# Kernel tuning notes

Measured on AMD Instinct MI355X. Metric: run time of the kernel, lower is better.

## Reference

```python
import jax, jax.numpy as jnp
import numpy as np
import math

# Poincare ball, curvature c=1 (fixed, requires_grad=False in source)
C = 1.0
SQC = math.sqrt(C)
EPS = 1e-15
BALL_EPS = 1e-5  # projection margin onto the open ball


def _beta(n):
    # B(n/2, 1/2) -- beta-concatenation scale from HNN++ (Shimizu et al.)
    return math.exp(math.lgamma(n / 2.0) + math.lgamma(0.5) - math.lgamma((n + 1) / 2.0))


def _project(x, axis):
    max_norm = (1.0 - BALL_EPS) / SQC
    n = jnp.linalg.norm(x, axis=axis, keepdims=True)
    return x * jnp.minimum(1.0, max_norm / jnp.maximum(n, EPS))


def _expmap0(v, axis):
    n = jnp.maximum(jnp.linalg.norm(v, axis=axis, keepdims=True), EPS)
    return _project(jnp.tanh(SQC * n) * v / (SQC * n), axis)


def _logmap0(x, axis):
    n = jnp.maximum(jnp.linalg.norm(x, axis=axis, keepdims=True), EPS)
    sn = jnp.minimum(SQC * n, 1.0 - 1e-7)
    return jnp.arctanh(sn) * x / (SQC * n)


def _hrelu(x, axis):
    # HReLU: relu in the tangent space at the origin
    return _expmap0(jax.nn.relu(_logmap0(x, axis)), axis)


def _poincare_fc(x, z, r):
    # Poincare fully-connected layer (HNN++): x [..., d_in], z [d_in, d_out], r [d_out]
    zn = jnp.maximum(jnp.linalg.norm(z, axis=0), EPS)        # [d_out]
    zu = z / zn                                               # unit columns
    cx2 = C * jnp.sum(x * x, axis=-1, keepdims=True)          # c*||x||^2
    drcr = 2.0 * SQC * r                                      # [d_out]
    # unidirectional Poincare MLR
    v = (2.0 * zn / SQC) * jnp.arcsinh(
        (2.0 * SQC * (x @ zu) * jnp.cosh(drcr) - (1.0 + cx2) * jnp.sinh(drcr))
        / jnp.maximum(1.0 - cx2, EPS)
    )
    # map generalized coordinates back onto the ball
    y = jnp.sinh(SQC * v) / SQC
    y = y / (1.0 + jnp.sqrt(1.0 + C * jnp.sum(y * y, axis=-1, keepdims=True)))
    return _project(y, -1)


def _hconv(x, z, r, k):
    # HConvolution2d: beta-concat unfold of kxk patches (man_dim = channels), then Poincare FC
    B, Cin, H, W = x.shape
    oh, ow = H - k + 1, W - k + 1
    v = _logmap0(x, axis=1) * (_beta(Cin * k * k) / _beta(Cin))
    # torch.F.unfold ordering: feature index = c*k*k + i*k + j
    patches = jnp.stack([v[:, :, i:i + oh, j:j + ow] for i in range(k) for j in range(k)], axis=2)
    p = patches.reshape(B, Cin * k * k, oh * ow)
    xp = _expmap0(p, axis=1).transpose(0, 2, 1)   # [B, L, Cin*k*k]
    out = _poincare_fc(xp, z, r)                  # [B, L, Cout]
    return out.transpose(0, 2, 1).reshape(B, -1, oh, ow)


def _hmaxpool2(x):
    # HMaxPool2d(kernel=2, stride=2): pick the patch element with max distance to origin
    # (distance is monotonic in the norm, so argmax over channel norm suffices)
    B, Cc, H, W = x.shape
    h, w = H // 2, W // 2
    xb = x.reshape(B, Cc, h, 2, w, 2).transpose(0, 2, 4, 1, 3, 5).reshape(B, h, w, Cc, 4)
    nb = jnp.sum(xb * xb, axis=3)                 # [B, h, w, 4] squared norms
    idx = jnp.argmax(nb, axis=-1)                 # [B, h, w]
    out = jnp.take_along_axis(xb, idx[..., None, None], axis=-1)[..., 0]  # [B, h, w, Cc]
    return out.transpose(0, 3, 1, 2)


def _hflatten(x):
    # ManifoldTensor.flatten(start_dim=1): beta-concatenation flatten (man_dim 1 -> last)
    B, Cin = x.shape[0], x.shape[1]
    n = x.shape[1] * x.shape[2] * x.shape[3]
    v = _logmap0(x, axis=1) * (_beta(n) / _beta(Cin))
    return _expmap0(v.reshape(B, n), axis=-1)


def setup_inputs() -> dict:
    key = jax.random.key(0)
    ks = jax.random.split(key, 12)
    B = 1024
    s = 0.05
    x = _expmap0(0.1 * jax.random.normal(ks[0], (B, 3, 32, 32), jnp.float32), axis=1)
    return {
        "x": x,
        "z1": s * jax.random.normal(ks[1], (75, 6), jnp.float32),    # 3*5*5 -> 6
        "b1": s * jax.random.normal(ks[2], (6,), jnp.float32),
        "z2": s * jax.random.normal(ks[3], (150, 16), jnp.float32),  # 6*5*5 -> 16
        "b2": s * jax.random.normal(ks[4], (16,), jnp.float32),
        "zf1": s * jax.random.normal(ks[5], (400, 120), jnp.float32),
        "bf1": s * jax.random.normal(ks[6], (120,), jnp.float32),
        "zf2": s * jax.random.normal(ks[7], (120, 84), jnp.float32),
        "bf2": s * jax.random.normal(ks[8], (84,), jnp.float32),
        "zf3": s * jax.random.normal(ks[9], (84, 10), jnp.float32),
        "bf3": s * jax.random.normal(ks[10], (10,), jnp.float32),
    }


def reference(x, z1, b1, z2, b2, zf1, bf1, zf2, bf2, zf3, bf3):
    h = _hmaxpool2(_hrelu(_hconv(x, z1, b1, 5), axis=1))    # [B,6,14,14]
    h = _hmaxpool2(_hrelu(_hconv(h, z2, b2, 5), axis=1))    # [B,16,5,5]
    h = _hflatten(h)                                         # [B,400]
    h = _hrelu(_poincare_fc(h, zf1, bf1), axis=-1)
    h = _hrelu(_poincare_fc(h, zf2, bf2), axis=-1)
    return _poincare_fc(h, zf3, bf3)                         # [B,10]
```

## Files before the change

### kernel.cpp

```cpp
#include <hip/hip_runtime.h>
#include <cmath>

#define EPSF 1e-15f
#define MAXN 0.99999f

#define OFF_ZU1  0
#define OFF_P1   512
#define OFF_ZU2  576
#define OFF_P2   3072
#define OFF_PF1  3200
#define OFF_PF2  3584
#define OFF_PF3  3904
#define OFF_BUF1 4096
#define OFF_BUF3 (OFF_BUF1 + 1204224)

__device__ __forceinline__ float fast_tanh_pos(float x) {
    float e = __expf(-2.0f * x);
    return (1.0f - e) / (1.0f + e);
}
__device__ __forceinline__ float fast_atanh01(float x) {
    return 0.5f * __logf((1.0f + x) / (1.0f - x));
}
__device__ __forceinline__ float sinh_k_asinh(float t, float k) {
    float at = fabsf(t);
    float lq = __logf(at + sqrtf(fmaf(at, at, 1.0f)));
    float p = __expf(k * lq);
    float r = 0.5f * (p - 1.0f / p);
    return t < 0.f ? -r : r;
}

__device__ __forceinline__ float wave_reduce_sum(float s) {
#pragma unroll
    for (int d = 1; d < 64; d <<= 1) s += __shfl_xor(s, d);
    return s;
}

__global__ __launch_bounds__(64) void prep_kernel(
        const float* __restrict__ z1, const float* __restrict__ r1,
        const float* __restrict__ z2, const float* __restrict__ r2,
        const float* __restrict__ zf1, const float* __restrict__ rf1,
        const float* __restrict__ zf2, const float* __restrict__ rf2,
        const float* __restrict__ zf3, const float* __restrict__ rf3,
        float* __restrict__ ws) {
    int blk = blockIdx.x, lane = threadIdx.x;
    const float* z; const float* r; int Din, Dout, o;
    float* zu = nullptr; float* par;
    if (blk < 6)        { z = z1;  r = r1;  Din = 75;  Dout = 6;   o = blk;       zu = ws + OFF_ZU1; par = ws + OFF_P1; }
    else if (blk < 22)  { z = z2;  r = r2;  Din = 150; Dout = 16;  o = blk - 6;   zu = ws + OFF_ZU2; par = ws + OFF_P2; }
    else if (blk < 142) { z = zf1; r = rf1; Din = 400; Dout = 120; o = blk - 22;  par = ws + OFF_PF1; }
    else if (blk < 226) { z = zf2; r = rf2; Din = 120; Dout = 84;  o = blk - 142; par = ws + OFF_PF2; }
    else                { z = zf3; r = rf3; Din = 84;  Dout = 10;  o = blk - 226; par = ws + OFF_PF3; }
    float s = 0.f;
    for (int f = lane; f < Din; f += 64) { float w = z[f * Dout + o]; s += w * w; }
    s = wave_reduce_sum(s);
    float zn = fmaxf(sqrtf(s), EPSF);
    if (lane == 0) {
        par[o] = zn;
        par[Dout + o]     = coshf(2.0f * r[o]);
        par[2 * Dout + o] = sinhf(2.0f * r[o]);
    }
    if (zu)
        for (int f = lane; f < Din; f += 64) zu[f * Dout + o] = z[f * Dout + o] / zn;
}

template<int N>
__device__ __forceinline__ float chain_fast(float (&a)[N], float n2,
        const float (&zn)[N], const float (&ch)[N], const float (&sh)[N]) {
    float nn = fmaxf(sqrtf(n2), EPSF);
    float t = fast_tanh_pos(nn);
    float s = t / nn * fminf(1.0f, MAXN / fmaxf(t, EPSF));
    float cx2 = (s * s) * n2;
    float denom = fmaxf(1.0f - cx2, EPSF);
    float ys2 = 0.f;
#pragma unroll
    for (int o = 0; o < N; o++) {
        float arg = (2.0f * (s * a[o]) * ch[o] - (1.0f + cx2) * sh[o]) / denom;
        float yy = sinh_k_asinh(arg, 2.0f * zn[o]);
        a[o] = yy; ys2 += yy * yy;
    }
    float dnm = 1.0f + sqrtf(1.0f + ys2);
    float ny2 = ys2 / (dnm * dnm);
    float ny = fmaxf(sqrtf(ny2), EPSF);
    float pf = fminf(1.0f, MAXN / ny);
    float sc = pf / dnm;
    float n2b = pf * pf * ny2;
    float nb = fmaxf(sqrtf(n2b), EPSF);
    float fb = fast_atanh01(fminf(nb, 1.0f - 1e-7f)) / nb;
    float m2 = 0.f;
#pragma unroll
    for (int o = 0; o < N; o++) { float uu = fmaxf(fb * sc * a[o], 0.f); a[o] = uu; m2 += uu * uu; }
    float m = fmaxf(sqrtf(m2), EPSF);
    float tm = fast_tanh_pos(m);
    float g = tm / m * fminf(1.0f, MAXN / fmaxf(tm, EPSF));
#pragma unroll
    for (int o = 0; o < N; o++) a[o] *= g;
    return g * g * m2;
}

__global__ __launch_bounds__(256) void conv1_kernel(const float* __restrict__ x,
        const float* __restrict__ ws, float* __restrict__ out, float ratio) {
    __shared__ float xv[3168];
    int b = blockIdx.x, tid = threadIdx.x;
    const float* zug  = ws + OFF_ZU1;
    const float* parg = ws + OFF_P1;
    for (int i = tid; i < 3072; i += 256) {
        int c = i >> 10, rem = i & 1023;
        xv[c * 1056 + (rem >> 5) * 33 + (rem & 31)] = x[(size_t)b * 3072 + i];
    }
    __syncthreads();
    for (int p = tid; p < 1024; p += 256) {
        int base = (p >> 5) * 33 + (p & 31);
        float a0 = xv[base], a1 = xv[1056 + base], a2 = xv[2112 + base];
        float n2 = a0 * a0 + a1 * a1 + a2 * a2;
        float nn = fmaxf(sqrtf(n2), EPSF);
        float f = fast_atanh01(fminf(nn, 1.0f - 1e-7f)) / nn * ratio;
        xv[base] = a0 * f; xv[1056 + base] = a1 * f; xv[2112 + base] = a2 * f;
    }
    __syncthreads();
    if (tid >= 196) return;
    int ph = tid / 14, pw = tid % 14;
    int base0 = (2 * ph) * 33 + 2 * pw;
    float acc[4][6], n2w[4];
#pragma unroll
    for (int wi = 0; wi < 4; wi++) {
        n2w[wi] = 0.f;
#pragma unroll
        for (int o = 0; o < 6; o++) acc[wi][o] = 0.f;
    }
#pragma unroll 1
    for (int c = 0; c < 3; c++) {
        float px[6][6];
#pragma unroll
        for (int r = 0; r < 6; r++)
#pragma unroll
        for (int j = 0; j < 6; j++)
            px[r][j] = xv[c * 1056 + base0 + r * 33 + j];
#pragma unroll
        for (int fi = 0; fi < 5; fi++) {
            const float* zp = zug + (c * 5 + fi) * 30;
#pragma unroll
            for (int fj = 0; fj < 5; fj++) {
                float zw[6];
#pragma unroll
                for (int o = 0; o < 6; o++) zw[o] = zp[fj * 6 + o];
#pragma unroll
                for (int dy = 0; dy < 2; dy++)
#pragma unroll
                for (int dx = 0; dx < 2; dx++) {
                    float v = px[fi + dy][fj + dx];
                    int wi = dy * 2 + dx;
                    n2w[wi] = fmaf(v, v, n2w[wi]);
#pragma unroll
                    for (int o = 0; o < 6; o++) acc[wi][o] = fmaf(v, zw[o], acc[wi][o]);
                }
            }
        }
    }
    float zn[6], chv[6], shv[6];
#pragma unroll
    for (int o = 0; o < 6; o++) { zn[o] = parg[o]; chv[o] = parg[6 + o]; shv[o] = parg[12 + o]; }
    float best[6]; float bestn = -1.f;
#pragma unroll
    for (int wi = 0; wi < 4; wi++) {
        float hn2 = chain_fast<6>(acc[wi], n2w[wi], zn, chv, shv);
        if (hn2 > bestn) {
            bestn = hn2;
#pragma unroll
            for (int o = 0; o < 6; o++) best[o] = acc[wi][o];
        }
    }
    float* op = out + (size_t)b * 1176 + tid;
#pragma unroll
    for (int o = 0; o < 6; o++) op[o * 196] = best[o];
}

__global__ __launch_bounds__(128) void conv2_kernel(const float* __restrict__ in,
        const float* __restrict__ ws, float* __restrict__ out,
        float ratio2, float ratio3) {
    __shared__ float xv[2522];
    int b0 = blockIdx.x * 2, tid = threadIdx.x;
    const float* zug  = ws + OFF_ZU2;
    const float* parg = ws + OFF_P2;
    for (int i = tid; i < 2352; i += 128) {
        int img = i / 1176, rem = i % 1176;
        int c = rem / 196, pix = rem % 196;
        xv[img * 1261 + c * 210 + (pix / 14) * 15 + pix % 14] = in[(size_t)b0 * 1176 + i];
    }
    __syncthreads();
    for (int t = tid; t < 392; t += 128) {
        int img = t / 196, pix = t % 196;
        int base = img * 1261 + (pix / 14) * 15 + pix % 14;
        float a[6]; float n2 = 0.f;
#pragma unroll
        for (int c = 0; c < 6; c++) { float v = xv[base + c * 210]; a[c] = v; n2 += v * v; }
        float nn = fmaxf(sqrtf(n2), EPSF);
        float f = fast_atanh01(fminf(nn, 1.0f - 1e-7f)) / nn * ratio2;
#pragma unroll
        for (int c = 0; c < 6; c++) xv[base + c * 210] = a[c] * f;
    }
    __syncthreads();
    int img = tid >> 6, l = tid & 63;
    int cell = l >> 1, h = l & 1;
    bool act = cell < 25;
    float best[8];
    float bestn = -1.f;
    float fcell = 0.f, part = 0.f;
    if (act) {
        int base0 = img * 1261 + (2 * (cell / 5)) * 15 + 2 * (cell % 5);
        float acc[4][8], n2w[4];
#pragma unroll
        for (int wi = 0; wi < 4; wi++) {
            n2w[wi] = 0.f;
#pragma unroll
            for (int o = 0; o < 8; o++) acc[wi][o] = 0.f;
        }
#pragma unroll 1
        for (int c = 0; c < 6; c++) {
            float px[6][6];
#pragma unroll
            for (int r = 0; r < 6; r++)
#pragma unroll
            for (int j = 0; j < 6; j++)
                px[r][j] = xv[base0 + c * 210 + r * 15 + j];
#pragma unroll
            for (int fi = 0; fi < 5; fi++) {
                const float* zp = zug + (c * 5 + fi) * 80 + 8 * h;
#pragma unroll
                for (int fj = 0; fj < 5; fj++) {
                    float zw[8];
#pragma unroll
                    for (int o = 0; o < 8; o++) zw[o] = zp[fj * 16 + o];
#pragma unroll
                    for (int dy = 0; dy < 2; dy++)
#pragma unroll
                    for (int dx = 0; dx < 2; dx++) {
                        float v = px[fi + dy][fj + dx];
                        int wi = dy * 2 + dx;
                        n2w[wi] = fmaf(v, v, n2w[wi]);
#pragma unroll
                        for (int o = 0; o < 8; o++) acc[wi][o] = fmaf(v, zw[o], acc[wi][o]);
                    }
                }
            }
        }
        float zn[8], chv[8], shv[8];
#pragma unroll
        for (int o = 0; o < 8; o++) {
            zn[o]  = parg[8 * h + o];
            chv[o] = parg[16 + 8 * h + o];
            shv[o] = parg[32 + 8 * h + o];
        }
#pragma unroll
        for (int wi = 0; wi < 4; wi++) {
            float nn = fmaxf(sqrtf(n2w[wi]), EPSF);
            float t = fast_tanh_pos(nn);
            float s = t / nn * fminf(1.0f, MAXN / fmaxf(t, EPSF));
            float cx2 = (s * s) * n2w[wi];
            float denom = fmaxf(1.0f - cx2, EPSF);
            float ys2h = 0.f;
#pragma unroll
            for (int o = 0; o < 8; o++) {
                float arg = (2.0f * (s * acc[wi][o]) * chv[o] - (1.0f + cx2) * shv[o]) / denom;
                float yy = sinh_k_asinh(arg, 2.0f * zn[o]);
                acc[wi][o] = yy; ys2h += yy * yy;
            }
            float ys2 = ys2h + __shfl_xor(ys2h, 1);
            float dnm = 1.0f + sqrtf(1.0f + ys2);
            float ny2 = ys2 / (dnm * dnm);
            float ny = fmaxf(sqrtf(ny2), EPSF);
            float pf = fminf(1.0f, MAXN / ny);
            float sc = pf / dnm;
            float n2b = pf * pf * ny2;
            float nb = fmaxf(sqrtf(n2b), EPSF);
            float fb = fast_atanh01(fminf(nb, 1.0f - 1e-7f)) / nb;
            float m2h = 0.f;
#pragma unroll
            for (int o = 0; o < 8; o++) { float uu = fmaxf(fb * sc * acc[wi][o], 0.f); acc[wi][o] = uu; m2h += uu * uu; }
            float m2 = m2h + __shfl_xor(m2h, 1);
            float m = fmaxf(sqrtf(m2), EPSF);
            float tm = fast_tanh_pos(m);
            float g = tm / m * fminf(1.0f, MAXN / fmaxf(tm, EPSF));
            float hn2 = g * g * m2;
            if (hn2 > bestn) {
                bestn = hn2;
#pragma unroll
                for (int o = 0; o < 8; o++) best[o] = g * acc[wi][o];
            }
        }
        float nn = fmaxf(sqrtf(bestn), EPSF);
        fcell = fast_atanh01(fminf(nn, 1.0f - 1e-7f)) / nn * ratio3;
        if (h == 0) part = fcell * fcell * bestn;
    }
    float s = wave_reduce_sum(part);
    float nn = fmaxf(sqrtf(s), EPSF);
    float t = fast_tanh_pos(nn);
    float g = t / nn * fminf(1.0f, MAXN / fmaxf(t, EPSF));
    if (act) {
        float* op = out + (size_t)(b0 + img) * 400 + cell;
#pragma unroll
        for (int o = 0; o < 8; o++) op[(8 * h + o) * 25] = g * fcell * best[o];
    }
}

template<int DIN, int DOUT>
__device__ __forceinline__ float dot_col(const float* __restrict__ xr,
        const float* __restrict__ z, int col) {
    float a0 = 0.f, a1 = 0.f, a2 = 0.f, a3 = 0.f;
    for (int f = 0; f < DIN; f += 4) {
        a0 = fmaf(xr[f],     z[(f)     * DOUT + col], a0);
        a1 = fmaf(xr[f + 1], z[(f + 1) * DOUT + col], a1);
        a2 = fmaf(xr[f + 2], z[(f + 2) * DOUT + col], a2);
        a3 = fmaf(xr[f + 3], z[(f + 3) * DOUT + col], a3);
    }
    return (a0 + a1) + (a2 + a3);
}

template<int DIN, int DOUT, bool RELU>
__device__ __forceinline__ float fc_layer_wave(int lane, const float* __restrict__ xr,
        float cx2, const float* __restrict__ z, const float* __restrict__ par,
        float* __restrict__ dst) {
    int o0 = lane, o1 = lane + 64;
    bool v0 = o0 < DOUT, v1 = o1 < DOUT;
    int c0 = v0 ? o0 : 0, c1 = v1 ? o1 : 0;
    float d0 = dot_col<DIN, DOUT>(xr, z, c0);
    float d1 = (DOUT > 64) ? dot_col<DIN, DOUT>(xr, z, c1) : 0.f;
    float denom = fmaxf(1.0f - cx2, EPSF);
    float zn0 = par[c0], ch0 = par[DOUT + c0], sh0 = par[2 * DOUT + c0];
    float arg0 = (2.0f * (d0 / zn0) * ch0 - (1.0f + cx2) * sh0) / denom;
    float y0 = sinh_k_asinh(arg0, 2.0f * zn0);
    float y1 = 0.f;
    if (DOUT > 64) {
        float zn1 = par[c1], ch1 = par[DOUT + c1], sh1 = par[2 * DOUT + c1];
        float arg1 = (2.0f * (d1 / zn1) * ch1 - (1.0f + cx2) * sh1) / denom;
        y1 = sinh_k_asinh(arg1, 2.0f * zn1);
    }
    float ys2 = wave_reduce_sum((v0 ? y0 * y0 : 0.f) + (v1 ? y1 * y1 : 0.f));
    float dnm = 1.0f + sqrtf(1.0f + ys2);
    float ny2 = ys2 / (dnm * dnm);
    float ny = fmaxf(sqrtf(ny2), EPSF);
    float pf = fminf(1.0f, MAXN / ny);
    float sc = pf / dnm;
    if (!RELU) {
        if (v0) dst[o0] = sc * y0;
        if (DOUT > 64 && v1) dst[o1] = sc * y1;
        return pf * pf * ny2;
    }
    float n2b = pf * pf * ny2;
    float nb = fmaxf(sqrtf(n2b), EPSF);
    float fb = fast_atanh01(fminf(nb, 1.0f - 1e-7f)) / nb;
    float u0 = fmaxf(fb * sc * y0, 0.f);
    float u1 = fmaxf(fb * sc * y1, 0.f);
    float m2 = wave_reduce_sum((v0 ? u0 * u0 : 0.f) + (v1 ? u1 * u1 : 0.f));
    float m = fmaxf(sqrtf(m2), EPSF);
    float tm = fast_tanh_pos(m);
    float g = tm / m * fminf(1.0f, MAXN / fmaxf(tm, EPSF));
    if (v0) dst[o0] = g * u0;
    if (DOUT > 64 && v1) dst[o1] = g * u1;
    return g * g * m2;
}

__global__ __launch_bounds__(256) void fc_stack_kernel(const float* __restrict__ in,
        const float* __restrict__ zf1, const float* __restrict__ zf2,
        const float* __restrict__ zf3, const float* __restrict__ ws,
        float* __restrict__ out) {
    __shared__ float xs[4][400];
    __shared__ float h1[4][120];
    __shared__ float h2[4][84];
    int wid = threadIdx.x >> 6, lane = threadIdx.x & 63;
    int b = blockIdx.x * 4 + wid;
    float* xr = xs[wid];
    float p = 0.f;
    for (int j = lane; j < 400; j += 64) { float v = in[(size_t)b * 400 + j]; xr[j] = v; p += v * v; }
    float cx2 = wave_reduce_sum(p);
    __syncthreads();
    float cx2b = fc_layer_wave<400, 120, true >(lane, xr,      cx2,  zf1, ws + OFF_PF1, h1[wid]);
    __syncthreads();
    float cx2c = fc_layer_wave<120, 84,  true >(lane, h1[wid], cx2b, zf2, ws + OFF_PF2, h2[wid]);
    __syncthreads();
    fc_layer_wave<84, 10, false>(lane, h2[wid], cx2c, zf3, ws + OFF_PF3, out + (size_t)b * 10);
}

static double beta_fn(double n) {
    return exp(lgamma(n / 2.0) + lgamma(0.5) - lgamma((n + 1) / 2.0));
}

extern "C" void kernel_launch(void* const* d_in, const int* in_sizes, int n_in,
                              void* d_out, int out_size, void* d_ws, size_t ws_size,
                              hipStream_t stream) {
    (void)in_sizes; (void)n_in; (void)out_size; (void)ws_size;
    const float* x   = (const float*)d_in[0];
    const float* z1  = (const float*)d_in[1];
    const float* b1  = (const float*)d_in[2];
    const float* z2  = (const float*)d_in[3];
    const float* b2  = (const float*)d_in[4];
    const float* zf1 = (const float*)d_in[5];
    const float* bf1 = (const float*)d_in[6];
    const float* zf2 = (const float*)d_in[7];
    const float* bf2 = (const float*)d_in[8];
    const float* zf3 = (const float*)d_in[9];
    const float* bf3 = (const float*)d_in[10];
    float* out = (float*)d_out;
    float* ws  = (float*)d_ws;

    const float ratio1 = (float)(beta_fn(75.0)  / beta_fn(3.0));
    const float ratio2 = (float)(beta_fn(150.0) / beta_fn(6.0));
    const float ratio3 = (float)(beta_fn(400.0) / beta_fn(16.0));

    float* buf1 = ws + OFF_BUF1;
    float* buf3 = ws + OFF_BUF3;

    prep_kernel<<<236, 64, 0, stream>>>(z1, b1, z2, b2, zf1, bf1, zf2, bf2, zf3, bf3, ws);
    conv1_kernel<<<1024, 256, 0, stream>>>(x, ws, buf1, ratio1);
    conv2_kernel<<<512, 128, 0, stream>>>(buf1, ws, buf3, ratio2, ratio3);
    fc_stack_kernel<<<256, 256, 0, stream>>>(buf3, zf1, zf2, zf3, ws, out);
}
```

Baseline: 182.9 us.

## Fuse conv1, conv2 and FC stack into one per-image mega kernel

Replaces the three-kernel pipeline (conv1, conv2, fc_stack) with a single kernel that processes one image per 256-thread block, keeping intermediates in shared memory instead of global buffers. Conv2 is restructured so each thread computes one output channel across a row of ten positions, with patch norms computed from precomputed row sums, and z2 staged in LDS. The FC layers now use the whole block with block-level reductions instead of one wave per image. This removes global round-trips and two launches, at the cost of larger LDS usage per block, more syncthreads, and lower parallelism in the FC phase (one image per block).

Result: faster. 175.8 us (-3.9%).

```diff
diff --git a/kernel.cpp b/kernel.cpp
--- a/kernel.cpp
+++ b/kernel.cpp
@@ -11,8 +11,6 @@
 #define OFF_PF1  3200
 #define OFF_PF2  3584
 #define OFF_PF3  3904
-#define OFF_BUF1 4096
-#define OFF_BUF3 (OFF_BUF1 + 1204224)
 
 __device__ __forceinline__ float fast_tanh_pos(float x) {
     float e = __expf(-2.0f * x);
@@ -33,6 +31,14 @@
 #pragma unroll
     for (int d = 1; d < 64; d <<= 1) s += __shfl_xor(s, d);
     return s;
+}
+
+__device__ __forceinline__ float block_reduce(float v, float* rbuf, int tid) {
+    float s = wave_reduce_sum(v);
+    __syncthreads();
+    if ((tid & 63) == 0) rbuf[tid >> 6] = s;
+    __syncthreads();
+    return rbuf[0] + rbuf[1] + rbuf[2] + rbuf[3];
 }
 
 __global__ __launch_bounds__(64) void prep_kernel(
@@ -97,139 +103,119 @@
     return g * g * m2;
 }
 
-__global__ __launch_bounds__(256) void conv1_kernel(const float* __restrict__ x,
-        const float* __restrict__ ws, float* __restrict__ out, float ratio) {
+template<int DIN, int DOUT, bool RELU>
+__device__ __forceinline__ float fc_block(int tid, const float* __restrict__ xin,
+        float gin, float cx2, const float* __restrict__ zg,
+        const float* __restrict__ parw, float* __restrict__ dst,
+        float* rbuf, float& gnext) {
+    constexpr int H = DIN / 2;
+    int col = tid >> 1, half = tid & 1;
+    bool act = tid < 2 * DOUT;
+    float d = 0.f;
+    if (act) {
+        float a0 = 0.f, a1 = 0.f;
+        int f0 = half * H;
+        for (int f = f0; f < f0 + H; f += 2) {
+            a0 = fmaf(xin[f],     zg[f * DOUT + col],       a0);
+            a1 = fmaf(xin[f + 1], zg[(f + 1) * DOUT + col], a1);
+        }
+        d = a0 + a1;
+    }
+    d += __shfl_xor(d, 1);
+    d *= gin;
+    float y = 0.f;
+    float denom = fmaxf(1.0f - cx2, EPSF);
+    if (act) {
+        float zn = parw[col], chv = parw[DOUT + col], shv = parw[2 * DOUT + col];
+        float arg = (2.0f * (d / zn) * chv - (1.0f + cx2) * shv) / denom;
+        y = sinh_k_asinh(arg, 2.0f * zn);
+    }
+    float ys2 = block_reduce((act && half == 0) ? y * y : 0.f, rbuf, tid);
+    float dnm = 1.0f + sqrtf(1.0f + ys2);
+    float ny2 = ys2 / (dnm * dnm);
+    float ny = fmaxf(sqrtf(ny2), EPSF);
+    float pf = fminf(1.0f, MAXN / ny);
+    float sc = pf / dnm;
+    if (!RELU) {
+        if (act && half == 0) dst[col] = sc * y;
+        gnext = 1.f;
+        return 0.f;
+    }
+    float n2b = pf * pf * ny2;
+    float nb = fmaxf(sqrtf(n2b), EPSF);
+    float fb = fast_atanh01(fminf(nb, 1.0f - 1e-7f)) / nb;
+    float u = fmaxf(fb * sc * y, 0.f);
+    if (act && half == 0) dst[col] = u;
+    float m2 = block_reduce((act && half == 0) ? u * u : 0.f, rbuf, tid);
+    float m = fmaxf(sqrtf(m2), EPSF);
+    float tm = fast_tanh_pos(m);
+    float g = tm / m * fminf(1.0f, MAXN / fmaxf(tm, EPSF));
+    gnext = g;
+    return g * g * m2;
+}
+
+__global__ __launch_bounds__(256) void mega_kernel(const float* __restrict__ x,
+        const float* __restrict__ ws, const float* __restrict__ zf1,
+        const float* __restrict__ zf2, const float* __restrict__ zf3,
+        float* __restrict__ out, float ratio1, float ratio2, float ratio3) {
     __shared__ float xv[3168];
+    __shared__ float z2s[2400];
+    __shared__ float par2[48];
+    __shared__ float v2[1260];
+    __shared__ float rs[140];
+    __shared__ float u3[400];
+    __shared__ float h1[120];
+    __shared__ float h2[84];
+    __shared__ float spart[5];
+    __shared__ float rbuf[4];
     int b = blockIdx.x, tid = threadIdx.x;
-    const float* zug  = ws + OFF_ZU1;
-    const float* parg = ws + OFF_P1;
+
     for (int i = tid; i < 3072; i += 256) {
         int c = i >> 10, rem = i & 1023;
         xv[c * 1056 + (rem >> 5) * 33 + (rem & 31)] = x[(size_t)b * 3072 + i];
     }
-    __syncthreads();
+    for (int i = tid; i < 2400; i += 256) z2s[i] = ws[OFF_ZU2 + i];
+    if (tid < 48) par2[tid] = ws[OFF_P2 + tid];
+    __syncthreads();
+
     for (int p = tid; p < 1024; p += 256) {
         int base = (p >> 5) * 33 + (p & 31);
         float a0 = xv[base], a1 = xv[1056 + base], a2 = xv[2112 + base];
         float n2 = a0 * a0 + a1 * a1 + a2 * a2;
         float nn = fmaxf(sqrtf(n2), EPSF);
-        float f = fast_atanh01(fminf(nn, 1.0f - 1e-7f)) / nn * ratio;
+        float f = fast_atanh01(fminf(nn, 1.0f - 1e-7f)) / nn * ratio1;
         xv[base] = a0 * f; xv[1056 + base] = a1 * f; xv[2112 + base] = a2 * f;
     }
     __syncthreads();
-    if (tid >= 196) return;
-    int ph = tid / 14, pw = tid % 14;
-    int base0 = (2 * ph) * 33 + 2 * pw;
-    float acc[4][6], n2w[4];
-#pragma unroll
-    for (int wi = 0; wi < 4; wi++) {
-        n2w[wi] = 0.f;
-#pragma unroll
-        for (int o = 0; o < 6; o++) acc[wi][o] = 0.f;
-    }
-#pragma unroll 1
-    for (int c = 0; c < 3; c++) {
-        float px[6][6];
-#pragma unroll
-        for (int r = 0; r < 6; r++)
-#pragma unroll
-        for (int j = 0; j < 6; j++)
-            px[r][j] = xv[c * 1056 + base0 + r * 33 + j];
-#pragma unroll
-        for (int fi = 0; fi < 5; fi++) {
-            const float* zp = zug + (c * 5 + fi) * 30;
-#pragma unroll
-            for (int fj = 0; fj < 5; fj++) {
-                float zw[6];
-#pragma unroll
-                for (int o = 0; o < 6; o++) zw[o] = zp[fj * 6 + o];
-#pragma unroll
-                for (int dy = 0; dy < 2; dy++)
-#pragma unroll
-                for (int dx = 0; dx < 2; dx++) {
-                    float v = px[fi + dy][fj + dx];
-                    int wi = dy * 2 + dx;
-                    n2w[wi] = fmaf(v, v, n2w[wi]);
-#pragma unroll
-                    for (int o = 0; o < 6; o++) acc[wi][o] = fmaf(v, zw[o], acc[wi][o]);
-                }
-            }
-        }
-    }
-    float zn[6], chv[6], shv[6];
-#pragma unroll
-    for (int o = 0; o < 6; o++) { zn[o] = parg[o]; chv[o] = parg[6 + o]; shv[o] = parg[12 + o]; }
-    float best[6]; float bestn = -1.f;
-#pragma unroll
-    for (int wi = 0; wi < 4; wi++) {
-        float hn2 = chain_fast<6>(acc[wi], n2w[wi], zn, chv, shv);
-        if (hn2 > bestn) {
-            bestn = hn2;
-#pragma unroll
-            for (int o = 0; o < 6; o++) best[o] = acc[wi][o];
-        }
-    }
-    float* op = out + (size_t)b * 1176 + tid;
-#pragma unroll
-    for (int o = 0; o < 6; o++) op[o * 196] = best[o];
-}
-
-__global__ __launch_bounds__(128) void conv2_kernel(const float* __restrict__ in,
-        const float* __restrict__ ws, float* __restrict__ out,
-        float ratio2, float ratio3) {
-    __shared__ float xv[2522];
-    int b0 = blockIdx.x * 2, tid = threadIdx.x;
-    const float* zug  = ws + OFF_ZU2;
-    const float* parg = ws + OFF_P2;
-    for (int i = tid; i < 2352; i += 128) {
-        int img = i / 1176, rem = i % 1176;
-        int c = rem / 196, pix = rem % 196;
-        xv[img * 1261 + c * 210 + (pix / 14) * 15 + pix % 14] = in[(size_t)b0 * 1176 + i];
-    }
-    __syncthreads();
-    for (int t = tid; t < 392; t += 128) {
-        int img = t / 196, pix = t % 196;
-        int base = img * 1261 + (pix / 14) * 15 + pix % 14;
-        float a[6]; float n2 = 0.f;
-#pragma unroll
-        for (int c = 0; c < 6; c++) { float v = xv[base + c * 210]; a[c] = v; n2 += v * v; }
-        float nn = fmaxf(sqrtf(n2), EPSF);
-        float f = fast_atanh01(fminf(nn, 1.0f - 1e-7f)) / nn * ratio2;
-#pragma unroll
-        for (int c = 0; c < 6; c++) xv[base + c * 210] = a[c] * f;
-    }
-    __syncthreads();
-    int img = tid >> 6, l = tid & 63;
-    int cell = l >> 1, h = l & 1;
-    bool act = cell < 25;
-    float best[8];
-    float bestn = -1.f;
-    float fcell = 0.f, part = 0.f;
-    if (act) {
-        int base0 = img * 1261 + (2 * (cell / 5)) * 15 + 2 * (cell % 5);
-        float acc[4][8], n2w[4];
+
+    if (tid < 196) {
+        const float* zug  = ws + OFF_ZU1;
+        const float* parg = ws + OFF_P1;
+        int ph = tid / 14, pw = tid % 14;
+        int base0 = (2 * ph) * 33 + 2 * pw;
+        float acc[4][6], n2w[4];
 #pragma unroll
         for (int wi = 0; wi < 4; wi++) {
             n2w[wi] = 0.f;
 #pragma unroll
-            for (int o = 0; o < 8; o++) acc[wi][o] = 0.f;
+            for (int o = 0; o < 6; o++) acc[wi][o] = 0.f;
         }
 #pragma unroll 1
-        for (int c = 0; c < 6; c++) {
+        for (int c = 0; c < 3; c++) {
             float px[6][6];
 #pragma unroll
             for (int r = 0; r < 6; r++)
 #pragma unroll
             for (int j = 0; j < 6; j++)
-                px[r][j] = xv[base0 + c * 210 + r * 15 + j];
+                px[r][j] = xv[c * 1056 + base0 + r * 33 + j];
 #pragma unroll
             for (int fi = 0; fi < 5; fi++) {
-                const float* zp = zug + (c * 5 + fi) * 80 + 8 * h;
+                const float* zp = zug + (c * 5 + fi) * 30;
 #pragma unroll
                 for (int fj = 0; fj < 5; fj++) {
-                    float zw[8];
-#pragma unroll
-                    for (int o = 0; o < 8; o++) zw[o] = zp[fj * 16 + o];
+                    float zw[6];
+#pragma unroll
+                    for (int o = 0; o < 6; o++) zw[o] = zp[fj * 6 + o];
 #pragma unroll
                     for (int dy = 0; dy < 2; dy++)
 #pragma unroll
@@ -238,33 +224,83 @@
                         int wi = dy * 2 + dx;
                         n2w[wi] = fmaf(v, v, n2w[wi]);
 #pragma unroll
-                        for (int o = 0; o < 8; o++) acc[wi][o] = fmaf(v, zw[o], acc[wi][o]);
+                        for (int o = 0; o < 6; o++) acc[wi][o] = fmaf(v, zw[o], acc[wi][o]);
                     }
                 }
             }
         }
-        float zn[8], chv[8], shv[8];
-#pragma unroll
-        for (int o = 0; o < 8; o++) {
-            zn[o]  = parg[8 * h + o];
-            chv[o] = parg[16 + 8 * h + o];
-            shv[o] = parg[32 + 8 * h + o];
-        }
+        float zn[6], chv[6], shv[6];
+#pragma unroll
+        for (int o = 0; o < 6; o++) { zn[o] = parg[o]; chv[o] = parg[6 + o]; shv[o] = parg[12 + o]; }
+        float best[6]; float bestn = -1.f;
 #pragma unroll
         for (int wi = 0; wi < 4; wi++) {
-            float nn = fmaxf(sqrtf(n2w[wi]), EPSF);
+            float hn2 = chain_fast<6>(acc[wi], n2w[wi], zn, chv, shv);
+            if (hn2 > bestn) {
+                bestn = hn2;
+#pragma unroll
+                for (int o = 0; o < 6; o++) best[o] = acc[wi][o];
+            }
+        }
+        float nn = fmaxf(sqrtf(bestn), EPSF);
+        float f2 = fast_atanh01(fminf(nn, 1.0f - 1e-7f)) / nn * ratio2;
+#pragma unroll
+        for (int o = 0; o < 6; o++) v2[o * 210 + ph * 15 + pw] = f2 * best[o];
+    }
+    __syncthreads();
+
+    if (tid < 140) {
+        int r = tid / 10, xq = tid % 10;
+        float ssum = 0.f;
+#pragma unroll
+        for (int c = 0; c < 6; c++)
+#pragma unroll
+        for (int j = 0; j < 5; j++) {
+            float v = v2[c * 210 + r * 15 + xq + j];
+            ssum = fmaf(v, v, ssum);
+        }
+        rs[tid] = ssum;
+    }
+    __syncthreads();
+
+    if (tid < 160) {
+        int wy = tid >> 4, o = tid & 15;
+        float acc[10];
+#pragma unroll
+        for (int w = 0; w < 10; w++) acc[w] = 0.f;
+#pragma unroll 1
+        for (int c = 0; c < 6; c++) {
+#pragma unroll 1
+            for (int fi = 0; fi < 5; fi++) {
+                float px[14];
+#pragma unroll
+                for (int k = 0; k < 14; k++) px[k] = v2[c * 210 + (wy + fi) * 15 + k];
+#pragma unroll
+                for (int fj = 0; fj < 5; fj++) {
+                    float zw = z2s[((c * 5 + fi) * 5 + fj) * 16 + o];
+#pragma unroll
+                    for (int w = 0; w < 10; w++)
+                        acc[w] = fmaf(px[w + fj], zw, acc[w]);
+                }
+            }
+        }
+        float znl = par2[o], chv = par2[16 + o], shv = par2[32 + o];
+        float val[10], hn2v[10];
+#pragma unroll
+        for (int w = 0; w < 10; w++) {
+            float n2 = rs[wy * 10 + w] + rs[(wy + 1) * 10 + w] + rs[(wy + 2) * 10 + w]
+                     + rs[(wy + 3) * 10 + w] + rs[(wy + 4) * 10 + w];
+            float nn = fmaxf(sqrtf(n2), EPSF);
             float t = fast_tanh_pos(nn);
             float s = t / nn * fminf(1.0f, MAXN / fmaxf(t, EPSF));
-            float cx2 = (s * s) * n2w[wi];
+            float cx2 = (s * s) * n2;
             float denom = fmaxf(1.0f - cx2, EPSF);
-            float ys2h = 0.f;
-#pragma unroll
-            for (int o = 0; o < 8; o++) {
-                float arg = (2.0f * (s * acc[wi][o]) * chv[o] - (1.0f + cx2) * shv[o]) / denom;
-                float yy = sinh_k_asinh(arg, 2.0f * zn[o]);
-                acc[wi][o] = yy; ys2h += yy * yy;
-            }
-            float ys2 = ys2h + __shfl_xor(ys2h, 1);
+            float arg = (2.0f * (s * acc[w]) * chv - (1.0f + cx2) * shv) / denom;
+            float y = sinh_k_asinh(arg, 2.0f * znl);
+            float p = y * y;
+#pragma unroll
+            for (int d = 1; d < 16; d <<= 1) p += __shfl_xor(p, d);
+            float ys2 = p;
             float dnm = 1.0f + sqrtf(1.0f + ys2);
             float ny2 = ys2 / (dnm * dnm);
             float ny = fmaxf(sqrtf(ny2), EPSF);
@@ -273,111 +309,50 @@
             float n2b = pf * pf * ny2;
             float nb = fmaxf(sqrtf(n2b), EPSF);
             float fb = fast_atanh01(fminf(nb, 1.0f - 1e-7f)) / nb;
-            float m2h = 0.f;
-#pragma unroll
-            for (int o = 0; o < 8; o++) { float uu = fmaxf(fb * sc * acc[wi][o], 0.f); acc[wi][o] = uu; m2h += uu * uu; }
-            float m2 = m2h + __shfl_xor(m2h, 1);
+            float u = fmaxf(fb * sc * y, 0.f);
+            float q = u * u;
+#pragma unroll
+            for (int d = 1; d < 16; d <<= 1) q += __shfl_xor(q, d);
+            float m2 = q;
             float m = fmaxf(sqrtf(m2), EPSF);
             float tm = fast_tanh_pos(m);
             float g = tm / m * fminf(1.0f, MAXN / fmaxf(tm, EPSF));
-            float hn2 = g * g * m2;
-            if (hn2 > bestn) {
-                bestn = hn2;
-#pragma unroll
-                for (int o = 0; o < 8; o++) best[o] = g * acc[wi][o];
+            val[w] = g * u;
+            hn2v[w] = g * g * m2;
+        }
+        float part = 0.f;
+#pragma unroll
+        for (int pw = 0; pw < 5; pw++) {
+            int i0 = 2 * pw, i1 = i0 + 1;
+            bool firstcol = hn2v[i0] >= hn2v[i1];
+            float iu = firstcol ? val[i0]  : val[i1];
+            float ih = firstcol ? hn2v[i0] : hn2v[i1];
+            float pu  = __shfl_xor(iu, 16);
+            float phh = __shfl_xor(ih, 16);
+            if ((wy & 1) == 0) {
+                bool top = ih >= phh;
+                float wu = top ? iu : pu;
+                float wh = top ? ih : phh;
+                float nn = fmaxf(sqrtf(wh), EPSF);
+                float f3 = fast_atanh01(fminf(nn, 1.0f - 1e-7f)) / nn * ratio3;
+                u3[o * 25 + (wy >> 1) * 5 + pw] = f3 * wu;
+                if (o == 0) part = fmaf(f3 * f3, wh, part);
             }
         }
-        float nn = fmaxf(sqrtf(bestn), EPSF);
-        fcell = fast_atanh01(fminf(nn, 1.0f - 1e-7f)) / nn * ratio3;
-        if (h == 0) part = fcell * fcell * bestn;
-    }
-    float s = wave_reduce_sum(part);
-    float nn = fmaxf(sqrtf(s), EPSF);
-    float t = fast_tanh_pos(nn);
-    float g = t / nn * fminf(1.0f, MAXN / fmaxf(t, EPSF));
-    if (act) {
-        float* op = out + (size_t)(b0 + img) * 400 + cell;
-#pragma unroll
-        for (int o = 0; o < 8; o++) op[(8 * h + o) * 25] = g * fcell * best[o];
-    }
-}
-
-template<int DIN, int DOUT>
-__device__ __forceinline__ float dot_col(const float* __restrict__ xr,
-        const float* __restrict__ z, int col) {
-    float a0 = 0.f, a1 = 0.f, a2 = 0.f, a3 = 0.f;
-    for (int f = 0; f < DIN; f += 4) {
-        a0 = fmaf(xr[f],     z[(f)     * DOUT + col], a0);
-        a1 = fmaf(xr[f + 1], z[(f + 1) * DOUT + col], a1);
-        a2 = fmaf(xr[f + 2], z[(f + 2) * DOUT + col], a2);
-        a3 = fmaf(xr[f + 3], z[(f + 3) * DOUT + col], a3);
-    }
-    return (a0 + a1) + (a2 + a3);
-}
-
-template<int DIN, int DOUT, bool RELU>
-__device__ __forceinline__ float fc_layer_wave(int lane, const float* __restrict__ xr,
-        float cx2, const float* __restrict__ z, const float* __restrict__ par,
-        float* __restrict__ dst) {
-    int o0 = lane, o1 = lane + 64;
-    bool v0 = o0 < DOUT, v1 = o1 < DOUT;
-    int c0 = v0 ? o0 : 0, c1 = v1 ? o1 : 0;
-    float d0 = dot_col<DIN, DOUT>(xr, z, c0);
-    float d1 = (DOUT > 64) ? dot_col<DIN, DOUT>(xr, z, c1) : 0.f;
-    float denom = fmaxf(1.0f - cx2, EPSF);
-    float zn0 = par[c0], ch0 = par[DOUT + c0], sh0 = par[2 * DOUT + c0];
-    float arg0 = (2.0f * (d0 / zn0) * ch0 - (1.0f + cx2) * sh0) / denom;
-    float y0 = sinh_k_asinh(arg0, 2.0f * zn0);
-    float y1 = 0.f;
-    if (DOUT > 64) {
-        float zn1 = par[c1], ch1 = par[DOUT + c1], sh1 = par[2 * DOUT + c1];
-        float arg1 = (2.0f * (d1 / zn1) * ch1 - (1.0f + cx2) * sh1) / denom;
-        y1 = sinh_k_asinh(arg1, 2.0f * zn1);
-    }
-    float ys2 = wave_reduce_sum((v0 ? y0 * y0 : 0.f) + (v1 ? y1 * y1 : 0.f));
-    float dnm = 1.0f + sqrtf(1.0f + ys2);
-    float ny2 = ys2 / (dnm * dnm);
-    float ny = fmaxf(sqrtf(ny2), EPSF);
-    float pf = fminf(1.0f, MAXN / ny);
-    float sc = pf / dnm;
-    if (!RELU) {
-        if (v0) dst[o0] = sc * y0;
-        if (DOUT > 64 && v1) dst[o1] = sc * y1;
-        return pf * pf * ny2;
-    }
-    float n2b = pf * pf * ny2;
-    float nb = fmaxf(sqrtf(n2b), EPSF);
-    float fb = fast_atanh01(fminf(nb, 1.0f - 1e-7f)) / nb;
-    float u0 = fmaxf(fb * sc * y0, 0.f);
-    float u1 = fmaxf(fb * sc * y1, 0.f);
-    float m2 = wave_reduce_sum((v0 ? u0 * u0 : 0.f) + (v1 ? u1 * u1 : 0.f));
-    float m = fmaxf(sqrtf(m2), EPSF);
-    float tm = fast_tanh_pos(m);
-    float g = tm / m * fminf(1.0f, MAXN / fmaxf(tm, EPSF));
-    if (v0) dst[o0] = g * u0;
-    if (DOUT > 64 && v1) dst[o1] = g * u1;
-    return g * g * m2;
-}
-
-__global__ __launch_bounds__(256) void fc_stack_kernel(const float* __restrict__ in,
-        const float* __restrict__ zf1, const float* __restrict__ zf2,
-        const float* __restrict__ zf3, const float* __restrict__ ws,
-        float* __restrict__ out) {
-    __shared__ float xs[4][400];
-    __shared__ float h1[4][120];
-    __shared__ float h2[4][84];
-    int wid = threadIdx.x >> 6, lane = threadIdx.x & 63;
-    int b = blockIdx.x * 4 + wid;
-    float* xr = xs[wid];
-    float p = 0.f;
-    for (int j = lane; j < 400; j += 64) { float v = in[(size_t)b * 400 + j]; xr[j] = v; p += v * v; }
-    float cx2 = wave_reduce_sum(p);
-    __syncthreads();
-    float cx2b = fc_layer_wave<400, 120, true >(lane, xr,      cx2,  zf1, ws + OFF_PF1, h1[wid]);
-    __syncthreads();
-    float cx2c = fc_layer_wave<120, 84,  true >(lane, h1[wid], cx2b, zf2, ws + OFF_PF2, h2[wid]);
-    __syncthreads();
-    fc_layer_wave<84, 10, false>(lane, h2[wid], cx2c, zf3, ws + OFF_PF3, out + (size_t)b * 10);
+        if ((wy & 1) == 0 && o == 0) spart[wy >> 1] = part;
+    }
+    __syncthreads();
+
+    float S = spart[0] + spart[1] + spart[2] + spart[3] + spart[4];
+    float nnS = fmaxf(sqrtf(S), EPSF);
+    float tS = fast_tanh_pos(nnS);
+    float gflat = tS / nnS * fminf(1.0f, MAXN / fmaxf(tS, EPSF));
+    float cx2a = gflat * gflat * S;
+
+    float g1, g2, gd;
+    float cx2b = fc_block<400, 120, true >(tid, u3, gflat, cx2a, zf1, ws + OFF_PF1, h1, rbuf, g1);
+    float cx2c = fc_block<120, 84,  true >(tid, h1, g1,   cx2b, zf2, ws + OFF_PF2, h2, rbuf, g2);
+    fc_block<84, 10, false>(tid, h2, g2, cx2c, zf3, ws + OFF_PF3, out + (size_t)b * 10, rbuf, gd);
 }
 
 static double beta_fn(double n) {
@@ -406,11 +381,7 @@
     const float ratio2 = (float)(beta_fn(150.0) / beta_fn(6.0));
     const float ratio3 = (float)(beta_fn(400.0) / beta_fn(16.0));
 
-    float* buf1 = ws + OFF_BUF1;
-    float* buf3 = ws + OFF_BUF3;
-
     prep_kernel<<<236, 64, 0, stream>>>(z1, b1, z2, b2, zf1, bf1, zf2, bf2, zf3, bf3, ws);
-    conv1_kernel<<<1024, 256, 0, stream>>>(x, ws, buf1, ratio1);
-    conv2_kernel<<<512, 128, 0, stream>>>(buf1, ws, buf3, ratio2, ratio3);
-    fc_stack_kernel<<<256, 256, 0, stream>>>(buf3, zf1, zf2, zf3, ws, out);
-}
+    mega_kernel<<<1024, 256, 0, stream>>>(x, ws, zf1, zf2, zf3, out,
+                                          ratio1, ratio2, ratio3);
+}
```
